# Kernel optimization log

Measured on AMD Instinct MI355X. Metric: run time of the kernel, lower is better.

The kernel has to match this reference:

```python
import jax, jax.numpy as jnp
import numpy as np

F, HE, HD, A = 128, 512, 512, 256
B, T = 32, 512

def _uniform(key, shape, k):
    return jax.random.uniform(key, shape, jnp.float32, -k, k)

def setup_inputs() -> dict:
    key = jax.random.key(0)
    ks = jax.random.split(key, 20)
    ke = 1.0 / np.sqrt(HE)
    kd = 1.0 / np.sqrt(HD)
    ka = 1.0 / np.sqrt(A)
    kf = 1.0 / np.sqrt(F)
    return {
        "x": jax.random.normal(ks[0], (B, T, F), jnp.float32),
        # encoder LSTM (torch gate order i,f,g,o)
        "enc_Wih": _uniform(ks[1], (4 * HE, F), ke),
        "enc_Whh": _uniform(ks[2], (4 * HE, HE), ke),
        "enc_bih": _uniform(ks[3], (4 * HE,), ke),
        "enc_bhh": _uniform(ks[4], (4 * HE,), ke),
        # attention
        "Wenc_w": _uniform(ks[5], (A, HE), 1.0 / np.sqrt(HE)),
        "Wenc_b": _uniform(ks[6], (A,), 1.0 / np.sqrt(HE)),
        "Wdec_w": _uniform(ks[7], (A, HD), kd),
        "Wdec_b": _uniform(ks[8], (A,), kd),
        "V_w": _uniform(ks[9], (1, A), ka),
        "V_b": _uniform(ks[10], (1,), ka),
        "attn_bias": _uniform(ks[11], (A,), kd),
        # decoder LSTMCell: input size HD+HE
        "dec_Wih": _uniform(ks[12], (4 * HD, HD + HE), kd),
        "dec_Whh": _uniform(ks[13], (4 * HD, HD), kd),
        "dec_bih": _uniform(ks[14], (4 * HD,), kd),
        "dec_bhh": _uniform(ks[15], (4 * HD,), kd),
    }

def _lstm_step(xw, h, c, Whh, bias, H):
    # xw = x @ Wih.T precomputed; bias = bih + bhh
    z = xw + h @ Whh.T + bias
    i, f, g, o = jnp.split(z, 4, axis=-1)
    i, f, o = jax.nn.sigmoid(i), jax.nn.sigmoid(f), jax.nn.sigmoid(o)
    g = jnp.tanh(g)
    c_new = f * c + i * g
    h_new = o * jnp.tanh(c_new)
    return h_new, c_new

def reference(x, enc_Wih, enc_Whh, enc_bih, enc_bhh,
              Wenc_w, Wenc_b, Wdec_w, Wdec_b, V_w, V_b, attn_bias,
              dec_Wih, dec_Whh, dec_bih, dec_bhh):
    nb, nt, _ = x.shape
    # ---- encoder LSTM ----
    xw = jnp.einsum('btf,gf->btg', x, enc_Wih)  # [B,T,4HE]
    enc_bias = enc_bih + enc_bhh
    def enc_step(carry, xw_t):
        h, c = carry
        h, c = _lstm_step(xw_t, h, c, enc_Whh, enc_bias, HE)
        return (h, c), h
    h0 = jnp.zeros((nb, HE), x.dtype)
    c0 = jnp.zeros((nb, HE), x.dtype)
    _, enc_states = jax.lax.scan(enc_step, (h0, c0), jnp.swapaxes(xw, 0, 1))
    enc_states = jnp.swapaxes(enc_states, 0, 1)  # [B,T,HE]

    # ---- initial decoder step: zero input, zero state ----
    dec_bias = dec_bih + dec_bhh
    z0 = jnp.broadcast_to(dec_bias, (nb, 4 * HD))
    i, f, g, o = jnp.split(z0, 4, axis=-1)
    cdec = jax.nn.sigmoid(i) * jnp.tanh(g)
    hdec = jax.nn.sigmoid(o) * jnp.tanh(cdec)

    # precompute encoder projection for attention (math identical to per-step)
    enc_proj = jnp.einsum('bte,ae->bta', enc_states, Wenc_w) + Wenc_b  # [B,T,A]

    def dec_step(carry, _):
        h, c = carry
        dscore = h @ Wdec_w.T + Wdec_b  # [B,A]
        align = jnp.tanh(enc_proj + dscore[:, None, :] + attn_bias)  # [B,T,A]
        logits = jnp.einsum('bta,a->bt', align, V_w[0]) + V_b[0]
        w = jax.nn.softmax(logits, axis=-1)  # [B,T]
        ctx = jnp.einsum('bt,bte->be', w, enc_states)  # [B,HE]
        dec_in = jnp.concatenate([ctx, h], axis=-1)
        h, c = _lstm_step(dec_in @ dec_Wih.T, h, c, dec_Whh, dec_bias, HD)
        return (h, c), h
    _, outs = jax.lax.scan(dec_step, (hdec, cdec), None, length=nt)
    return jnp.swapaxes(outs, 0, 1)  # [B,T,HD]
```

## Files before the change

kernel.cpp:

```cpp
#include <hip/hip_runtime.h>
#include <stdint.h>

#define DEV __device__ __forceinline__

namespace {

constexpr int kT = 512, kB = 32, kF = 128, kHE = 512, kHD = 512, kA = 256;

typedef _Float16 f16;
typedef _Float16 h4 __attribute__((ext_vector_type(4)));
typedef unsigned long long u64;

constexpr size_t oWdecC  = 0;
constexpr size_t oWdWH   = oWdecC + 1048576;
constexpr size_t oEncSt  = oWdWH + 65536;
constexpr size_t oEncPr  = oEncSt + (size_t)kB*kT*kHE;
constexpr size_t oHdec   = oEncPr + (size_t)kB*kT*kA;
constexpr size_t oCtx    = oHdec + 3ull*kB*kHD;
constexpr size_t oDen    = oCtx + 3ull*kB*kHE;
constexpr size_t oScp    = oDen + 96;
constexpr size_t oEbias  = oScp + (size_t)kB*16*kA;
constexpr size_t oDbias  = oEbias + 2048;
constexpr size_t oAb2    = oDbias + 2048;
constexpr size_t oCtr    = oAb2 + 256;
constexpr size_t oHenc   = oCtr + 2048;
constexpr size_t oCtxP   = oEncSt;
constexpr size_t oDenP   = oEncSt + 3ull*32*16*512;

constexpr float kScale = 1.0f/64.0f;

DEV float frcp(float x){ return __builtin_amdgcn_rcpf(x); }
DEV float fsig(float x){ return frcp(1.f + __expf(-x)); }
DEV float ftanh(float x){ return 1.f - 2.f*frcp(__expf(2.f*x) + 1.f); }

DEV float ld_na(const float* p){ return __hip_atomic_load((float*)p, __ATOMIC_RELAXED, __HIP_MEMORY_SCOPE_AGENT); }
DEV void  st_na(float* p, float v){ __hip_atomic_store(p, v, __ATOMIC_RELAXED, __HIP_MEMORY_SCOPE_AGENT); }
DEV int   ld_ni(const int* p){ return __hip_atomic_load((int*)p, __ATOMIC_RELAXED, __HIP_MEMORY_SCOPE_AGENT); }
DEV void  st_ni(int* p, int v){ __hip_atomic_store(p, v, __ATOMIC_RELAXED, __HIP_MEMORY_SCOPE_AGENT); }
DEV float2 ld_na2(const float* p){
  u64 v = __hip_atomic_load((const u64*)p, __ATOMIC_RELAXED, __HIP_MEMORY_SCOPE_AGENT);
  union { u64 u; float2 f; } cv; cv.u = v; return cv.f;
}
DEV void st_na2(float* p, float2 v){
  union { float2 f; u64 u; } cv; cv.f = v;
  __hip_atomic_store((u64*)p, cv.u, __ATOMIC_RELAXED, __HIP_MEMORY_SCOPE_AGENT);
}

DEV void wait_slots(const int* base, int cnt, int tgt, int* abortf){
  if (threadIdx.x < 64){
    int lane = threadIdx.x;
    int guard = 0;
    for (;;){
      int ok = 1;
      for (int i = lane; i < cnt; i += 64) ok &= (ld_ni(base + i) >= tgt);
      if (__all(ok)) break;
      if (ld_ni(abortf) != 0) break;
      if (++guard > (1<<21)){ st_ni(abortf, 1); break; }
      __builtin_amdgcn_s_sleep(1);
    }
  }
  __syncthreads();
}
DEV void wait_count(const int* p, int tgt, int* abortf){
  if (threadIdx.x < 64){
    int guard = 0;
    for (;;){
      if (ld_ni(p) >= tgt) break;
      if (ld_ni(abortf) != 0) break;
      if (++guard > (1<<21)){ st_ni(abortf, 1); break; }
      __builtin_amdgcn_s_sleep(2);
    }
  }
  __syncthreads();
}
DEV void stamp_slot(int* slot, int v){
  __syncthreads();
  if (threadIdx.x == 0) st_ni(slot, v);
}

}

__global__ __launch_bounds__(256) void init_kernel(
    const float* __restrict__ eBih, const float* __restrict__ eBhh,
    const float* __restrict__ WdecW, const float* __restrict__ WdecB, const float* __restrict__ attnB,
    const float* __restrict__ dWih, const float* __restrict__ dWhh,
    const float* __restrict__ dBih, const float* __restrict__ dBhh,
    float* __restrict__ ws)
{
  float* whc = ws + oWdecC;
  f16* wdwh  = (f16*)(ws + oWdWH);
  float* hdec  = ws + oHdec;
  float* ctxb  = ws + oCtx;
  float* den   = ws + oDen;
  float* ebias = ws + oEbias;
  float* dbias = ws + oDbias;
  float* ab2w  = ws + oAb2;
  float* henc  = ws + oHenc;
  const int gid = blockIdx.x*256 + threadIdx.x;
  const int stride = gridDim.x*256;
  for (int i=gid; i<2048*512; i+=stride){
    int col = i>>9, k = i&511;
    whc[i] = dWih[((size_t)col<<10) + 512 + k] + dWhh[((size_t)col<<9) + k];
  }
  for (int i=gid; i<256*512; i+=stride)  wdwh[i] = (f16)WdecW[i];
  for (int i=gid; i<2048; i+=stride){ ebias[i] = eBih[i]+eBhh[i]; dbias[i] = dBih[i]+dBhh[i]; }
  for (int i=gid; i<256; i+=stride)  ab2w[i] = WdecB[i]+attnB[i];
  for (int i=gid; i<3*kB*kHE; i+=stride) ctxb[i] = 0.f;
  for (int i=gid; i<2*kB*kHE; i+=stride) henc[i] = 0.f;
  for (int i=gid; i<96; i+=stride) den[i] = 0.f;
  for (int i=gid; i<kB*kHD; i+=stride){
    int e = i & 511;
    float zi = dBih[e]+dBhh[e];
    float zg = dBih[1024+e]+dBhh[1024+e];
    float zo = dBih[1536+e]+dBhh[1536+e];
    float c0 = fsig(zi)*ftanh(zg);
    hdec[i] = fsig(zo)*ftanh(c0);
  }
}

__global__ __launch_bounds__(256, 1) void enc_kernel(
    const float* __restrict__ x, const float* __restrict__ eWih,
    const float* __restrict__ eWhh, float* __restrict__ ws)
{
  constexpr int WP = 644;
  constexpr int XP = 648;
  __shared__ float wsm[32*WP];
  __shared__ float xh[8*XP];
  __shared__ float zs[8][32];
  const float* ebias = ws + oEbias;
  float* encst = ws + oEncSt;
  float* henc  = ws + oHenc;
  int* ctr = (int*)(ws + oCtr);
  int* abortf = ctr;
  int* slotE = ctr + 1600;

  const int tid = threadIdx.x, bid = blockIdx.x;
  const int q = bid >> 6, j = bid & 63;
  const int b0 = q*8, e0 = j*8;

  for (int i = tid; i < 32*640; i += 256){
    int r = i / 640, k = i - r*640;
    int gate = r >> 3, el = r & 7;
    int grow = gate*kHE + e0 + el;
    float v = (k < kF) ? eWih[(size_t)grow*kF + k] : eWhh[(size_t)grow*kHE + (k - kF)];
    wsm[r*WP + k] = v;
  }
  const int b_l = tid >> 5, row = tid & 31;
  const float biasr = ebias[(row>>3)*kHE + e0 + (row&7)];
  const int b_p = tid >> 3, e_p = tid & 7;
  float creg = 0.f;
  __syncthreads();

  int p = 0;
  for (int t = 0; t < kT; ++t){
    if (tid < 256){
      int bl2 = tid >> 5, q4 = tid & 31;
      *(float4*)(&xh[bl2*XP + 4*q4]) = ((const float4*)(x + ((size_t)(b0+bl2)*kT + t)*kF))[q4];
    }
    wait_slots(slotE + q*64, 64, t, abortf);
    #pragma unroll
    for (int i = 0; i < 4; ++i){
      int idx = tid + 256*i;
      int bl2 = idx >> 7, q4 = idx & 127;
      const float* hsrc = henc + (size_t)p*kB*kHE + (size_t)(b0+bl2)*kHE + 4*q4;
      float4 hv;
      hv.x = ld_na(hsrc); hv.y = ld_na(hsrc+1); hv.z = ld_na(hsrc+2); hv.w = ld_na(hsrc+3);
      *(float4*)(&xh[bl2*XP + kF + 4*q4]) = hv;
    }
    __syncthreads();
    {
      const float4* wr = (const float4*)(&wsm[row*WP]);
      const float4* xr = (const float4*)(&xh[b_l*XP]);
      float a0=0.f, a1=0.f, a2=0.f, a3=0.f;
      #pragma unroll 8
      for (int kq = 0; kq < 160; ++kq){
        float4 w = wr[kq], v = xr[kq];
        a0 += w.x*v.x; a1 += w.y*v.y; a2 += w.z*v.z; a3 += w.w*v.w;
      }
      zs[b_l][row] = (a0+a1)+(a2+a3) + biasr;
    }
    __syncthreads();
    if (tid < 64){
      float zi = zs[b_p][0*8 + e_p];
      float zf = zs[b_p][1*8 + e_p];
      float zg = zs[b_p][2*8 + e_p];
      float zo = zs[b_p][3*8 + e_p];
      float c2 = fsig(zf)*creg + fsig(zi)*ftanh(zg);
      creg = c2;
      float h = fsig(zo)*ftanh(c2);
      int b = b0 + b_p, e = e0 + e_p;
      st_na(&henc[(size_t)(p^1)*kB*kHE + (size_t)b*kHE + e], h);
      encst[((size_t)b*kT + t)*kHE + e] = h;
    }
    stamp_slot(&slotE[q*64 + j], t+1);
    p ^= 1;
  }
}

__global__ __launch_bounds__(256) void encproj_kernel(
    const float* __restrict__ WencW, const float* __restrict__ WencB,
    float* __restrict__ ws)
{
  const float* encst = ws + oEncSt;
  float* encpr = ws + oEncPr;
  __shared__ float4 et[32][32];
  const int tid = threadIdx.x, bid = blockIdx.x;
  const int r0 = bid*32;
  float acc[32];
  #pragma unroll
  for (int i=0;i<32;++i) acc[i]=0.f;
  for (int kt=0; kt<4; ++kt){
    #pragma unroll
    for (int i2=0;i2<4;++i2){
      int q = tid + i2*256;
      int row = q>>5, qi = q&31;
      et[row][qi] = ((const float4*)(encst + ((size_t)(r0+row))*kHE + kt*128))[qi];
    }
    __syncthreads();
    const float4* wv = (const float4*)(WencW + (size_t)tid*kHE + kt*128);
    #pragma unroll 1
    for (int q=0;q<32;++q){
      float4 w = wv[q];
      #pragma unroll
      for (int i=0;i<32;++i){
        float4 e4 = et[i][q];
        acc[i] += e4.x*w.x + e4.y*w.y + e4.z*w.z + e4.w*w.w;
      }
    }
    __syncthreads();
  }
  float bb = WencB[tid];
  #pragma unroll
  for (int i=0;i<32;++i) encpr[((size_t)(r0+i))*kA + tid] = acc[i] + bb;
}

namespace {
struct SA  { float h[32]; float sc[256]; float lw[32]; };
struct SC  { float xt[16][260]; float zb[128][2]; };
struct __align__(16) SmemDec {
  float wsl[8][1028];
  float v[256];
  union { SA a; SC c; } u;
};
}

__global__ __launch_bounds__(256, 2) void dec_kernel(
    const float* __restrict__ Vw, const float* __restrict__ dWih,
    float* __restrict__ out, float* __restrict__ ws)
{
  __shared__ SmemDec sm;
  const int tid = threadIdx.x, bid = blockIdx.x;
  const float* whc = ws + oWdecC;
  const f16* wdwh  = (const f16*)(ws + oWdWH);
  const float* encst = ws + oEncSt;
  const float* encpr = ws + oEncPr;
  float* hdec = ws + oHdec;
  float* ctxb = ws + oCtx;
  float* den  = ws + oDen;
  float* scp  = ws + oScp;
  float* ctxp = ws + oCtxP;
  float* denp = ws + oDenP;
  const float* dbias = ws + oDbias;
  const float* ab2w  = ws + oAb2;
  int* ctr   = (int*)(ws + oCtr);
  int* abortf = ctr;
  int* startc = ctr + 16;
  int* slotC = ctr + 64;
  int* slotA = ctr + 576;
  int* slotB = ctr + 1088;
  int* slotR = ctr + 1856;

  const int bA = bid >> 4, tc = bid & 15, t0a = tc*32;
  const int half = bid >> 8, ecp = bid & 255, e0c = ecp*2;
  const bool isR = (tc == 0);
  const int col_l = tid & 127, ksC = tid >> 7;
  const int e_lC = col_l & 1, gateC = (col_l>>1)&3, b_lC = col_l>>3;
  const int wrow = gateC*2 + e_lC;

  for (int i = tid; i < 8*1024; i += 256){
    int rr = i >> 10, k = i & 1023;
    int col = (rr>>1)*kHD + e0c + (rr&1);
    float v = (k < 512) ? dWih[(size_t)col*1024 + k] : whc[(size_t)col*512 + (k-512)];
    sm.wsl[rr][k] = v;
  }
  sm.v[tid] = Vw[tid];

  h4 wA[8];
  { const h4* wv0 = (const h4*)(wdwh + (size_t)tid*kHD + t0a);
    #pragma unroll
    for (int q=0;q<8;++q) wA[q] = wv0[q]; }
  const int tl = tid>>3, as = tid&7;
  float4 eprR[8];
  { const float* eb2 = encpr + ((size_t)bA*kT + t0a + tl)*kA + as*4;
    #pragma unroll
    for (int q=0;q<8;++q) eprR[q] = *(const float4*)(eb2 + q*32); }
  float2 ev[32];
  { const float* eb = encst + ((size_t)bA*kT + t0a)*kHE + 2*tid;
    #pragma unroll
    for (int j=0;j<32;++j) ev[j] = *(const float2*)(eb + (size_t)j*kHE); }

  const float ab2r = ab2w[tid];
  float cregD=0, dbi=0, dbf=0, dbg=0, dbo=0;
  if (tid < 32){
    int e = e0c + (tid&1);
    dbi = dbias[e]; dbf = dbias[512+e]; dbg = dbias[1024+e]; dbo = dbias[1536+e];
    cregD = fsig(dbi)*ftanh(dbg);
  }
  __syncthreads();
  if (tid == 0) atomicAdd(startc, 1);
  wait_count(startc, 512, abortf);

  int r = 0;
  for (int t=0; t<kT; ++t){
    const int rn = (r==2) ? 0 : r+1;
    wait_slots(slotC + (bA>>4)*256 + tc*16, 16, t, abortf);
    if (tid < 32) sm.u.a.h[tid] = ld_na(hdec + (size_t)r*kB*kHD + (size_t)bA*kHD + t0a + tid);
    __syncthreads();
    {
      float sp = 0.f;
      #pragma unroll
      for (int q=0;q<8;++q){
        h4 w = wA[q];
        sp += (float)w.x*sm.u.a.h[q*4+0] + (float)w.y*sm.u.a.h[q*4+1]
            + (float)w.z*sm.u.a.h[q*4+2] + (float)w.w*sm.u.a.h[q*4+3];
      }
      st_na(&scp[((size_t)bA*16 + tc)*kA + tid], sp);
    }
    stamp_slot(&slotA[bA*16 + tc], t+1);
    wait_slots(slotA + bA*16, 16, t+1, abortf);
    {
      float sc = ab2r;
      #pragma unroll
      for (int j=0;j<16;++j) sc += ld_na(&scp[((size_t)bA*16 + j)*kA + tid]);
      sm.u.a.sc[tid] = sc;
    }
    __syncthreads();
    {
      float acc = 0.f;
      #pragma unroll
      for (int q=0;q<8;++q){
        int a0 = q*32 + as*4;
        float4 e4 = eprR[q];
        acc += sm.v[a0+0]*ftanh(e4.x + sm.u.a.sc[a0+0]);
        acc += sm.v[a0+1]*ftanh(e4.y + sm.u.a.sc[a0+1]);
        acc += sm.v[a0+2]*ftanh(e4.z + sm.u.a.sc[a0+2]);
        acc += sm.v[a0+3]*ftanh(e4.w + sm.u.a.sc[a0+3]);
      }
      acc += __shfl_down(acc, 4, 8);
      acc += __shfl_down(acc, 2, 8);
      acc += __shfl_down(acc, 1, 8);
      if (as == 0) sm.u.a.lw[tl] = __expf(acc) * kScale;
    }
    __syncthreads();
    {
      float c0=0.f, c1=0.f;
      #pragma unroll
      for (int j=0;j<32;++j){
        float w = sm.u.a.lw[j];
        c0 += w*ev[j].x; c1 += w*ev[j].y;
      }
      st_na2(&ctxp[(((size_t)r*kB + bA)*16 + tc)*kHE + 2*tid], make_float2(c0, c1));
      if (tid == 0){
        float ds = 0.f;
        #pragma unroll
        for (int j=0;j<32;++j) ds += sm.u.a.lw[j];
        st_na(&denp[((size_t)r*kB + bA)*16 + tc], ds);
      }
    }
    stamp_slot(&slotB[bA*16 + tc], t+1);
    if (isR){
      wait_slots(slotB + bA*16, 16, t+1, abortf);
      {
        const float* pb = ctxp + ((size_t)r*kB + bA)*16*kHE + 2*tid;
        float s0=0.f, s1=0.f;
        #pragma unroll
        for (int j=0;j<16;++j){
          float2 p = ld_na2(pb + (size_t)j*kHE);
          s0 += p.x; s1 += p.y;
        }
        st_na2(&ctxb[((size_t)r*kB + bA)*kHE + 2*tid], make_float2(s0, s1));
        float d = (tid < 16) ? ld_na(&denp[((size_t)r*kB + bA)*16 + tid]) : 0.f;
        d += __shfl_down(d, 8, 16);
        d += __shfl_down(d, 4, 16);
        d += __shfl_down(d, 2, 16);
        d += __shfl_down(d, 1, 16);
        if (tid == 0) st_na(&den[r*kB + bA], d);
      }
      stamp_slot(&slotR[bA], t+1);
    }
    wait_slots(slotR + half*16, 16, t+1, abortf);
    {
      const float rv = frcp(ld_na(&den[r*kB + half*16 + b_lC]));
      const float* cbase = ctxb + (size_t)r*kB*kHE + (size_t)(half*16)*kHE + 2*tid;
      const float* hbase = hdec + (size_t)r*kB*kHD + (size_t)(half*16)*kHD + 2*tid;
      float2 cu[16], hu[16];
      #pragma unroll
      for (int b=0;b<16;++b) cu[b] = ld_na2(cbase + (size_t)b*kHE);
      const int off  = (2*tid) & 255;
      const int mych = tid >> 7;
      float accc=0.f, acch=0.f;
      #pragma unroll
      for (int kc=0; kc<4; ++kc){
        if (kc == 1){
          #pragma unroll
          for (int b=0;b<16;++b) hu[b] = ld_na2(hbase + (size_t)b*kHD);
        }
        if ((kc & 1) == mych){
          #pragma unroll
          for (int b=0;b<16;++b)
            *(float2*)(&sm.u.c.xt[b][off]) = (kc < 2) ? cu[b] : hu[b];
        }
        __syncthreads();
        {
          const float4* wc4 = (const float4*)(&sm.wsl[wrow][kc*256 + ksC*128]);
          const float4* xv  = (const float4*)(&sm.u.c.xt[b_lC][ksC*128]);
          float a0=0.f, a1=0.f, a2=0.f, a3=0.f;
          #pragma unroll 8
          for (int q=0;q<32;++q){
            float4 w = wc4[q], v = xv[q];
            a0 += w.x*v.x; a1 += w.y*v.y; a2 += w.z*v.z; a3 += w.w*v.w;
          }
          float a = (a0+a1)+(a2+a3);
          if (kc < 2) accc += a; else acch += a;
        }
        __syncthreads();
      }
      sm.u.c.zb[col_l][ksC] = accc*rv + acch;
      __syncthreads();
      if (tid < 32){
        int base = (tid>>1)*8 + (tid&1);
        int e = e0c + (tid&1), b2 = half*16 + (tid>>1);
        float zi = sm.u.c.zb[base+0][0] + sm.u.c.zb[base+0][1] + dbi;
        float zf = sm.u.c.zb[base+2][0] + sm.u.c.zb[base+2][1] + dbf;
        float zg = sm.u.c.zb[base+4][0] + sm.u.c.zb[base+4][1] + dbg;
        float zo = sm.u.c.zb[base+6][0] + sm.u.c.zb[base+6][1] + dbo;
        float c2 = fsig(zf)*cregD + fsig(zi)*ftanh(zg);
        cregD = c2;
        float h = fsig(zo)*ftanh(c2);
        st_na(&hdec[(size_t)rn*kB*kHD + (size_t)b2*kHD + e], h);
        out[((size_t)b2*kT + t)*kHD + e] = h;
      }
    }
    stamp_slot(&slotC[half*256 + ecp], t+1);
    r = rn;
  }
}

extern "C" void kernel_launch(void* const* d_in, const int* in_sizes, int n_in,
                              void* d_out, int out_size, void* d_ws, size_t ws_size,
                              hipStream_t stream) {
  (void)in_sizes; (void)n_in; (void)out_size; (void)ws_size;
  const float* x     = (const float*)d_in[0];
  const float* eWih  = (const float*)d_in[1];
  const float* eWhh  = (const float*)d_in[2];
  const float* eBih  = (const float*)d_in[3];
  const float* eBhh  = (const float*)d_in[4];
  const float* WencW = (const float*)d_in[5];
  const float* WencB = (const float*)d_in[6];
  const float* WdecW = (const float*)d_in[7];
  const float* WdecB = (const float*)d_in[8];
  const float* Vw    = (const float*)d_in[9];
  const float* attnB = (const float*)d_in[11];
  const float* dWih  = (const float*)d_in[12];
  const float* dWhh  = (const float*)d_in[13];
  const float* dBih  = (const float*)d_in[14];
  const float* dBhh  = (const float*)d_in[15];
  float* ws = (float*)d_ws;
  int* ctr = (int*)(ws + oCtr);
  hipMemsetAsync(ctr, 0, 8192, stream);
  hipLaunchKernelGGL(init_kernel, dim3(512), dim3(256), 0, stream,
                     eBih, eBhh, WdecW, WdecB, attnB, dWih, dWhh, dBih, dBhh, ws);
  hipLaunchKernelGGL(enc_kernel, dim3(256), dim3(256), 0, stream, x, eWih, eWhh, ws);
  hipLaunchKernelGGL(encproj_kernel, dim3(512), dim3(256), 0, stream, WencW, WencB, ws);
  hipLaunchKernelGGL(dec_kernel, dim3(512), dim3(256), 0, stream, Vw, dWih, (float*)d_out, ws);
}
```

Measured before the change: 15.27 ms.

## Replace slot-counter barriers with tagged 64-bit value/step words for hidden-state handoff

```diff
diff --git a/kernel.cpp b/kernel.cpp
--- a/kernel.cpp
+++ b/kernel.cpp
@@ -14,18 +14,18 @@
 constexpr size_t oWdecC  = 0;
 constexpr size_t oWdWH   = oWdecC + 1048576;
 constexpr size_t oEncSt  = oWdWH + 65536;
-constexpr size_t oEncPr  = oEncSt + (size_t)kB*kT*kHE;
-constexpr size_t oHdec   = oEncPr + (size_t)kB*kT*kA;
-constexpr size_t oCtx    = oHdec + 3ull*kB*kHD;
-constexpr size_t oDen    = oCtx + 3ull*kB*kHE;
-constexpr size_t oScp    = oDen + 96;
-constexpr size_t oEbias  = oScp + (size_t)kB*16*kA;
+constexpr size_t oEncPr  = oEncSt + 8388608;
+constexpr size_t oHseq   = oEncPr + 4194304;
+constexpr size_t oEbias  = oHseq + 98304;
 constexpr size_t oDbias  = oEbias + 2048;
 constexpr size_t oAb2    = oDbias + 2048;
 constexpr size_t oCtr    = oAb2 + 256;
 constexpr size_t oHenc   = oCtr + 2048;
-constexpr size_t oCtxP   = oEncSt;
-constexpr size_t oDenP   = oEncSt + 3ull*32*16*512;
+constexpr size_t aCtxP   = oEncSt;
+constexpr size_t aScp    = aCtxP + 786432;
+constexpr size_t aCtxB   = aScp + 131072;
+constexpr size_t aDsp    = aCtxB + 49152;
+constexpr size_t aDen    = aDsp + 1536;
 
 constexpr float kScale = 1.0f/64.0f;
 
@@ -37,6 +37,8 @@
 DEV void  st_na(float* p, float v){ __hip_atomic_store(p, v, __ATOMIC_RELAXED, __HIP_MEMORY_SCOPE_AGENT); }
 DEV int   ld_ni(const int* p){ return __hip_atomic_load((int*)p, __ATOMIC_RELAXED, __HIP_MEMORY_SCOPE_AGENT); }
 DEV void  st_ni(int* p, int v){ __hip_atomic_store(p, v, __ATOMIC_RELAXED, __HIP_MEMORY_SCOPE_AGENT); }
+DEV u64   ld_nt(const u64* p){ return __hip_atomic_load((u64*)p, __ATOMIC_RELAXED, __HIP_MEMORY_SCOPE_AGENT); }
+DEV void  st_nt(u64* p, u64 v){ __hip_atomic_store(p, v, __ATOMIC_RELAXED, __HIP_MEMORY_SCOPE_AGENT); }
 DEV float2 ld_na2(const float* p){
   u64 v = __hip_atomic_load((const u64*)p, __ATOMIC_RELAXED, __HIP_MEMORY_SCOPE_AGENT);
   union { u64 u; float2 f; } cv; cv.u = v; return cv.f;
@@ -45,6 +47,10 @@
   union { float2 f; u64 u; } cv; cv.f = v;
   __hip_atomic_store((u64*)p, cv.u, __ATOMIC_RELAXED, __HIP_MEMORY_SCOPE_AGENT);
 }
+
+DEV u64 pk(float v, int tag){ union{float f; uint32_t u;} c; c.f = v; return ((u64)(uint32_t)tag << 32) | (u64)c.u; }
+DEV float payf(u64 x){ union{uint32_t u; float f;} c; c.u = (uint32_t)x; return c.f; }
+DEV int   ptag(u64 x){ return (int)(x >> 32); }
 
 DEV void wait_slots(const int* base, int cnt, int tgt, int* abortf){
   if (threadIdx.x < 64){
@@ -89,13 +95,11 @@
 {
   float* whc = ws + oWdecC;
   f16* wdwh  = (f16*)(ws + oWdWH);
-  float* hdec  = ws + oHdec;
-  float* ctxb  = ws + oCtx;
-  float* den   = ws + oDen;
+  u64* hseq  = (u64*)(ws + oHseq);
+  u64* henc  = (u64*)(ws + oHenc);
   float* ebias = ws + oEbias;
   float* dbias = ws + oDbias;
   float* ab2w  = ws + oAb2;
-  float* henc  = ws + oHenc;
   const int gid = blockIdx.x*256 + threadIdx.x;
   const int stride = gridDim.x*256;
   for (int i=gid; i<2048*512; i+=stride){
@@ -105,17 +109,16 @@
   for (int i=gid; i<256*512; i+=stride)  wdwh[i] = (f16)WdecW[i];
   for (int i=gid; i<2048; i+=stride){ ebias[i] = eBih[i]+eBhh[i]; dbias[i] = dBih[i]+dBhh[i]; }
   for (int i=gid; i<256; i+=stride)  ab2w[i] = WdecB[i]+attnB[i];
-  for (int i=gid; i<3*kB*kHE; i+=stride) ctxb[i] = 0.f;
-  for (int i=gid; i<2*kB*kHE; i+=stride) henc[i] = 0.f;
-  for (int i=gid; i<96; i+=stride) den[i] = 0.f;
+  for (int i=gid; i<2*kB*kHE; i+=stride) henc[i] = 0ull;
   for (int i=gid; i<kB*kHD; i+=stride){
     int e = i & 511;
     float zi = dBih[e]+dBhh[e];
     float zg = dBih[1024+e]+dBhh[1024+e];
     float zo = dBih[1536+e]+dBhh[1536+e];
     float c0 = fsig(zi)*ftanh(zg);
-    hdec[i] = fsig(zo)*ftanh(c0);
-  }
+    hseq[i] = pk(fsig(zo)*ftanh(c0), 0);
+  }
+  for (int i=gid; i<2*kB*kHD; i+=stride) hseq[kB*kHD + i] = 0ull;
 }
 
 __global__ __launch_bounds__(256, 1) void enc_kernel(
@@ -129,10 +132,9 @@
   __shared__ float zs[8][32];
   const float* ebias = ws + oEbias;
   float* encst = ws + oEncSt;
-  float* henc  = ws + oHenc;
+  u64* hq = (u64*)(ws + oHenc);
   int* ctr = (int*)(ws + oCtr);
   int* abortf = ctr;
-  int* slotE = ctr + 1600;
 
   const int tid = threadIdx.x, bid = blockIdx.x;
   const int q = bid >> 6, j = bid & 63;
@@ -153,19 +155,31 @@
 
   int p = 0;
   for (int t = 0; t < kT; ++t){
-    if (tid < 256){
+    __syncthreads();
+    {
       int bl2 = tid >> 5, q4 = tid & 31;
       *(float4*)(&xh[bl2*XP + 4*q4]) = ((const float4*)(x + ((size_t)(b0+bl2)*kT + t)*kF))[q4];
     }
-    wait_slots(slotE + q*64, 64, t, abortf);
-    #pragma unroll
-    for (int i = 0; i < 4; ++i){
-      int idx = tid + 256*i;
-      int bl2 = idx >> 7, q4 = idx & 127;
-      const float* hsrc = henc + (size_t)p*kB*kHE + (size_t)(b0+bl2)*kHE + 4*q4;
-      float4 hv;
-      hv.x = ld_na(hsrc); hv.y = ld_na(hsrc+1); hv.z = ld_na(hsrc+2); hv.w = ld_na(hsrc+3);
-      *(float4*)(&xh[bl2*XP + kF + 4*q4]) = hv;
+    {
+      u64 gv[16];
+      int guard = 0;
+      for (;;){
+        bool ok = true;
+        #pragma unroll
+        for (int i2=0;i2<16;++i2){
+          int idx = tid + 256*i2; int bl2 = idx>>9, col = idx&511;
+          gv[i2] = ld_nt(&hq[(size_t)p*kB*kHE + (size_t)(b0+bl2)*kHE + col]);
+          ok &= (ptag(gv[i2]) >= t);
+        }
+        if (__all((int)ok)) break;
+        if (ld_ni(abortf) != 0) break;
+        if (++guard > (1<<20)){ st_ni(abortf, 1); break; }
+      }
+      #pragma unroll
+      for (int i2=0;i2<16;++i2){
+        int idx = tid + 256*i2; int bl2 = idx>>9, col = idx&511;
+        xh[bl2*XP + kF + col] = payf(gv[i2]);
+      }
     }
     __syncthreads();
     {
@@ -189,10 +203,9 @@
       creg = c2;
       float h = fsig(zo)*ftanh(c2);
       int b = b0 + b_p, e = e0 + e_p;
-      st_na(&henc[(size_t)(p^1)*kB*kHE + (size_t)b*kHE + e], h);
+      st_nt(&hq[(size_t)(p^1)*kB*kHE + (size_t)b*kHE + e], pk(h, t+1));
       encst[((size_t)b*kT + t)*kHE + e] = h;
     }
-    stamp_slot(&slotE[q*64 + j], t+1);
     p ^= 1;
   }
 }
@@ -254,18 +267,17 @@
   const f16* wdwh  = (const f16*)(ws + oWdWH);
   const float* encst = ws + oEncSt;
   const float* encpr = ws + oEncPr;
-  float* hdec = ws + oHdec;
-  float* ctxb = ws + oCtx;
-  float* den  = ws + oDen;
-  float* scp  = ws + oScp;
-  float* ctxp = ws + oCtxP;
-  float* denp = ws + oDenP;
+  u64* hseq = (u64*)(ws + oHseq);
+  float* ctxp = ws + aCtxP;
+  float* scp  = ws + aScp;
+  float* ctxb = ws + aCtxB;
+  float* dsp  = ws + aDsp;
+  float* den  = ws + aDen;
   const float* dbias = ws + oDbias;
   const float* ab2w  = ws + oAb2;
   int* ctr   = (int*)(ws + oCtr);
   int* abortf = ctr;
-  int* startc = ctr + 16;
-  int* slotC = ctr + 64;
+  int* gate1 = ctr + 16;
   int* slotA = ctr + 576;
   int* slotB = ctr + 1088;
   int* slotR = ctr + 1856;
@@ -307,14 +319,24 @@
     cregD = fsig(dbi)*ftanh(dbg);
   }
   __syncthreads();
-  if (tid == 0) atomicAdd(startc, 1);
-  wait_count(startc, 512, abortf);
+  if (tid == 0) atomicAdd(gate1, 1);
+  wait_count(gate1, 512, abortf);
+
+  const int off  = (2*tid) & 255;
+  const int mych = tid >> 7;
 
   int r = 0;
   for (int t=0; t<kT; ++t){
     const int rn = (r==2) ? 0 : r+1;
-    wait_slots(slotC + (bA>>4)*256 + tc*16, 16, t, abortf);
-    if (tid < 32) sm.u.a.h[tid] = ld_na(hdec + (size_t)r*kB*kHD + (size_t)bA*kHD + t0a + tid);
+    __syncthreads();
+    if (tid < 32){
+      const u64* hp = hseq + ((size_t)r*kB + bA)*kHE + t0a + tid;
+      u64 v; int guard = 0;
+      for (;;){ v = ld_nt(hp); if (ptag(v) >= t) break;
+                if (ld_ni(abortf) != 0) break;
+                if (++guard > (1<<20)){ st_ni(abortf,1); break; } }
+      sm.u.a.h[tid] = payf(v);
+    }
     __syncthreads();
     {
       float sp = 0.f;
@@ -364,7 +386,7 @@
         float ds = 0.f;
         #pragma unroll
         for (int j=0;j<32;++j) ds += sm.u.a.lw[j];
-        st_na(&denp[((size_t)r*kB + bA)*16 + tc], ds);
+        st_na(&dsp[((size_t)r*kB + bA)*16 + tc], ds);
       }
     }
     stamp_slot(&slotB[bA*16 + tc], t+1);
@@ -379,7 +401,7 @@
           s0 += p.x; s1 += p.y;
         }
         st_na2(&ctxb[((size_t)r*kB + bA)*kHE + 2*tid], make_float2(s0, s1));
-        float d = (tid < 16) ? ld_na(&denp[((size_t)r*kB + bA)*16 + tid]) : 0.f;
+        float d = (tid < 16) ? ld_na(&dsp[((size_t)r*kB + bA)*16 + tid]) : 0.f;
         d += __shfl_down(d, 8, 16);
         d += __shfl_down(d, 4, 16);
         d += __shfl_down(d, 2, 16);
@@ -392,23 +414,26 @@
     {
       const float rv = frcp(ld_na(&den[r*kB + half*16 + b_lC]));
       const float* cbase = ctxb + (size_t)r*kB*kHE + (size_t)(half*16)*kHE + 2*tid;
-      const float* hbase = hdec + (size_t)r*kB*kHD + (size_t)(half*16)*kHD + 2*tid;
-      float2 cu[16], hu[16];
-      #pragma unroll
-      for (int b=0;b<16;++b) cu[b] = ld_na2(cbase + (size_t)b*kHE);
-      const int off  = (2*tid) & 255;
-      const int mych = tid >> 7;
+      const u64*   hbase = hseq + ((size_t)r*kB + half*16)*kHE + 2*tid;
+      float cux[16], cuy[16], hux[16], huy[16];
+      #pragma unroll
+      for (int b=0;b<16;++b){
+        float2 cv = ld_na2(cbase + (size_t)b*kHE);
+        cux[b] = cv.x; cuy[b] = cv.y;
+        hux[b] = payf(ld_nt(hbase + (size_t)b*kHE));
+        huy[b] = payf(ld_nt(hbase + (size_t)b*kHE + 1));
+      }
       float accc=0.f, acch=0.f;
       #pragma unroll
       for (int kc=0; kc<4; ++kc){
-        if (kc == 1){
-          #pragma unroll
-          for (int b=0;b<16;++b) hu[b] = ld_na2(hbase + (size_t)b*kHD);
-        }
         if ((kc & 1) == mych){
-          #pragma unroll
-          for (int b=0;b<16;++b)
-            *(float2*)(&sm.u.c.xt[b][off]) = (kc < 2) ? cu[b] : hu[b];
+          if (kc < 2){
+            #pragma unroll
+            for (int b=0;b<16;++b){ sm.u.c.xt[b][off] = cux[b]; sm.u.c.xt[b][off+1] = cuy[b]; }
+          } else {
+            #pragma unroll
+            for (int b=0;b<16;++b){ sm.u.c.xt[b][off] = hux[b]; sm.u.c.xt[b][off+1] = huy[b]; }
+          }
         }
         __syncthreads();
         {
@@ -437,11 +462,10 @@
         float c2 = fsig(zf)*cregD + fsig(zi)*ftanh(zg);
         cregD = c2;
         float h = fsig(zo)*ftanh(c2);
-        st_na(&hdec[(size_t)rn*kB*kHD + (size_t)b2*kHD + e], h);
+        st_nt(&hseq[((size_t)rn*kB + b2)*kHD + e], pk(h, t+1));
         out[((size_t)b2*kT + t)*kHD + e] = h;
       }
     }
-    stamp_slot(&slotC[half*256 + ecp], t+1);
     r = rn;
   }
 }
```

Result: slower. 18.91 ms (+23.8%).

## Compute decoder h-part of gate GEMV before waiting on context reduction

Applied to the files above, without the earlier changes.

```diff
diff --git a/kernel.cpp b/kernel.cpp
--- a/kernel.cpp
+++ b/kernel.cpp
@@ -90,8 +90,6 @@
   float* whc = ws + oWdecC;
   f16* wdwh  = (f16*)(ws + oWdWH);
   float* hdec  = ws + oHdec;
-  float* ctxb  = ws + oCtx;
-  float* den   = ws + oDen;
   float* ebias = ws + oEbias;
   float* dbias = ws + oDbias;
   float* ab2w  = ws + oAb2;
@@ -105,9 +103,7 @@
   for (int i=gid; i<256*512; i+=stride)  wdwh[i] = (f16)WdecW[i];
   for (int i=gid; i<2048; i+=stride){ ebias[i] = eBih[i]+eBhh[i]; dbias[i] = dBih[i]+dBhh[i]; }
   for (int i=gid; i<256; i+=stride)  ab2w[i] = WdecB[i]+attnB[i];
-  for (int i=gid; i<3*kB*kHE; i+=stride) ctxb[i] = 0.f;
   for (int i=gid; i<2*kB*kHE; i+=stride) henc[i] = 0.f;
-  for (int i=gid; i<96; i+=stride) den[i] = 0.f;
   for (int i=gid; i<kB*kHD; i+=stride){
     int e = i & 511;
     float zi = dBih[e]+dBhh[e];
@@ -153,7 +149,7 @@
 
   int p = 0;
   for (int t = 0; t < kT; ++t){
-    if (tid < 256){
+    {
       int bl2 = tid >> 5, q4 = tid & 31;
       *(float4*)(&xh[bl2*XP + 4*q4]) = ((const float4*)(x + ((size_t)(b0+bl2)*kT + t)*kF))[q4];
     }
@@ -240,7 +236,8 @@
 struct __align__(16) SmemDec {
   float wsl[8][1028];
   float v[256];
-  union { SA a; SC c; } u;
+  SA a;
+  SC c;
 };
 }
 
@@ -310,19 +307,22 @@
   if (tid == 0) atomicAdd(startc, 1);
   wait_count(startc, 512, abortf);
 
+  const int off  = (2*tid) & 255;
+  const int mych = tid >> 7;
+
   int r = 0;
   for (int t=0; t<kT; ++t){
     const int rn = (r==2) ? 0 : r+1;
     wait_slots(slotC + (bA>>4)*256 + tc*16, 16, t, abortf);
-    if (tid < 32) sm.u.a.h[tid] = ld_na(hdec + (size_t)r*kB*kHD + (size_t)bA*kHD + t0a + tid);
+    if (tid < 32) sm.a.h[tid] = ld_na(hdec + (size_t)r*kB*kHD + (size_t)bA*kHD + t0a + tid);
     __syncthreads();
     {
       float sp = 0.f;
       #pragma unroll
       for (int q=0;q<8;++q){
         h4 w = wA[q];
-        sp += (float)w.x*sm.u.a.h[q*4+0] + (float)w.y*sm.u.a.h[q*4+1]
-            + (float)w.z*sm.u.a.h[q*4+2] + (float)w.w*sm.u.a.h[q*4+3];
+        sp += (float)w.x*sm.a.h[q*4+0] + (float)w.y*sm.a.h[q*4+1]
+            + (float)w.z*sm.a.h[q*4+2] + (float)w.w*sm.a.h[q*4+3];
       }
       st_na(&scp[((size_t)bA*16 + tc)*kA + tid], sp);
     }
@@ -332,7 +332,7 @@
       float sc = ab2r;
       #pragma unroll
       for (int j=0;j<16;++j) sc += ld_na(&scp[((size_t)bA*16 + j)*kA + tid]);
-      sm.u.a.sc[tid] = sc;
+      sm.a.sc[tid] = sc;
     }
     __syncthreads();
     {
@@ -341,29 +341,29 @@
       for (int q=0;q<8;++q){
         int a0 = q*32 + as*4;
         float4 e4 = eprR[q];
-        acc += sm.v[a0+0]*ftanh(e4.x + sm.u.a.sc[a0+0]);
-        acc += sm.v[a0+1]*ftanh(e4.y + sm.u.a.sc[a0+1]);
-        acc += sm.v[a0+2]*ftanh(e4.z + sm.u.a.sc[a0+2]);
-        acc += sm.v[a0+3]*ftanh(e4.w + sm.u.a.sc[a0+3]);
+        acc += sm.v[a0+0]*ftanh(e4.x + sm.a.sc[a0+0]);
+        acc += sm.v[a0+1]*ftanh(e4.y + sm.a.sc[a0+1]);
+        acc += sm.v[a0+2]*ftanh(e4.z + sm.a.sc[a0+2]);
+        acc += sm.v[a0+3]*ftanh(e4.w + sm.a.sc[a0+3]);
       }
       acc += __shfl_down(acc, 4, 8);
       acc += __shfl_down(acc, 2, 8);
       acc += __shfl_down(acc, 1, 8);
-      if (as == 0) sm.u.a.lw[tl] = __expf(acc) * kScale;
+      if (as == 0) sm.a.lw[tl] = __expf(acc) * kScale;
     }
     __syncthreads();
     {
       float c0=0.f, c1=0.f;
       #pragma unroll
       for (int j=0;j<32;++j){
-        float w = sm.u.a.lw[j];
+        float w = sm.a.lw[j];
         c0 += w*ev[j].x; c1 += w*ev[j].y;
       }
       st_na2(&ctxp[(((size_t)r*kB + bA)*16 + tc)*kHE + 2*tid], make_float2(c0, c1));
       if (tid == 0){
         float ds = 0.f;
         #pragma unroll
-        for (int j=0;j<32;++j) ds += sm.u.a.lw[j];
+        for (int j=0;j<32;++j) ds += sm.a.lw[j];
         st_na(&denp[((size_t)r*kB + bA)*16 + tc], ds);
       }
     }
@@ -388,52 +388,77 @@
       }
       stamp_slot(&slotR[bA], t+1);
     }
-    wait_slots(slotR + half*16, 16, t+1, abortf);
-    {
-      const float rv = frcp(ld_na(&den[r*kB + half*16 + b_lC]));
-      const float* cbase = ctxb + (size_t)r*kB*kHE + (size_t)(half*16)*kHE + 2*tid;
+    wait_slots(slotC + half*256, 256, t, abortf);
+    float acch = 0.f;
+    {
       const float* hbase = hdec + (size_t)r*kB*kHD + (size_t)(half*16)*kHD + 2*tid;
-      float2 cu[16], hu[16];
-      #pragma unroll
-      for (int b=0;b<16;++b) cu[b] = ld_na2(cbase + (size_t)b*kHE);
-      const int off  = (2*tid) & 255;
-      const int mych = tid >> 7;
-      float accc=0.f, acch=0.f;
-      #pragma unroll
-      for (int kc=0; kc<4; ++kc){
-        if (kc == 1){
-          #pragma unroll
-          for (int b=0;b<16;++b) hu[b] = ld_na2(hbase + (size_t)b*kHD);
-        }
+      float hux[16], huy[16];
+      #pragma unroll
+      for (int b=0;b<16;++b){
+        float2 hv = ld_na2(hbase + (size_t)b*kHD);
+        hux[b] = hv.x; huy[b] = hv.y;
+      }
+      #pragma unroll
+      for (int kc=2; kc<4; ++kc){
         if ((kc & 1) == mych){
           #pragma unroll
-          for (int b=0;b<16;++b)
-            *(float2*)(&sm.u.c.xt[b][off]) = (kc < 2) ? cu[b] : hu[b];
+          for (int b=0;b<16;++b){ sm.c.xt[b][off] = hux[b]; sm.c.xt[b][off+1] = huy[b]; }
         }
         __syncthreads();
         {
           const float4* wc4 = (const float4*)(&sm.wsl[wrow][kc*256 + ksC*128]);
-          const float4* xv  = (const float4*)(&sm.u.c.xt[b_lC][ksC*128]);
+          const float4* xv  = (const float4*)(&sm.c.xt[b_lC][ksC*128]);
           float a0=0.f, a1=0.f, a2=0.f, a3=0.f;
           #pragma unroll 8
           for (int q=0;q<32;++q){
             float4 w = wc4[q], v = xv[q];
             a0 += w.x*v.x; a1 += w.y*v.y; a2 += w.z*v.z; a3 += w.w*v.w;
           }
-          float a = (a0+a1)+(a2+a3);
-          if (kc < 2) accc += a; else acch += a;
+          acch += (a0+a1)+(a2+a3);
         }
         __syncthreads();
       }
-      sm.u.c.zb[col_l][ksC] = accc*rv + acch;
+    }
+    wait_slots(slotR + half*16, 16, t+1, abortf);
+    {
+      const float rv = frcp(ld_na(&den[r*kB + half*16 + b_lC]));
+      const float* cbase = ctxb + (size_t)r*kB*kHE + (size_t)(half*16)*kHE + 2*tid;
+      float cux[16], cuy[16];
+      #pragma unroll
+      for (int b=0;b<16;++b){
+        float2 cv = ld_na2(cbase + (size_t)b*kHE);
+        cux[b] = cv.x; cuy[b] = cv.y;
+      }
+      float accc = 0.f;
+      #pragma unroll
+      for (int kc=0; kc<2; ++kc){
+        if ((kc & 1) == mych){
+          #pragma unroll
+          for (int b=0;b<16;++b){ sm.c.xt[b][off] = cux[b]; sm.c.xt[b][off+1] = cuy[b]; }
+        }
+        __syncthreads();
+        {
+          const float4* wc4 = (const float4*)(&sm.wsl[wrow][kc*256 + ksC*128]);
+          const float4* xv  = (const float4*)(&sm.c.xt[b_lC][ksC*128]);
+          float a0=0.f, a1=0.f, a2=0.f, a3=0.f;
+          #pragma unroll 8
+          for (int q=0;q<32;++q){
+            float4 w = wc4[q], v = xv[q];
+            a0 += w.x*v.x; a1 += w.y*v.y; a2 += w.z*v.z; a3 += w.w*v.w;
+          }
+          accc += (a0+a1)+(a2+a3);
+        }
+        __syncthreads();
+      }
+      sm.c.zb[col_l][ksC] = accc*rv + acch;
       __syncthreads();
       if (tid < 32){
         int base = (tid>>1)*8 + (tid&1);
         int e = e0c + (tid&1), b2 = half*16 + (tid>>1);
-        float zi = sm.u.c.zb[base+0][0] + sm.u.c.zb[base+0][1] + dbi;
-        float zf = sm.u.c.zb[base+2][0] + sm.u.c.zb[base+2][1] + dbf;
-        float zg = sm.u.c.zb[base+4][0] + sm.u.c.zb[base+4][1] + dbg;
-        float zo = sm.u.c.zb[base+6][0] + sm.u.c.zb[base+6][1] + dbo;
+        float zi = sm.c.zb[base+0][0] + sm.c.zb[base+0][1] + dbi;
+        float zf = sm.c.zb[base+2][0] + sm.c.zb[base+2][1] + dbf;
+        float zg = sm.c.zb[base+4][0] + sm.c.zb[base+4][1] + dbg;
+        float zo = sm.c.zb[base+6][0] + sm.c.zb[base+6][1] + dbo;
         float c2 = fsig(zf)*cregD + fsig(zi)*ftanh(zg);
         cregD = c2;
         float h = fsig(zo)*ftanh(c2);
```

Measured after the change: 14.98 ms. About the same (-1.9%).
